# Kernel tuning notes

Measured on AMD Instinct MI355X. Metric: run time of the kernel, lower is better.

The kernel has to match this reference:

```python
import jax, jax.numpy as jnp
import numpy as np

E, S, L, H, C = 32, 64, 20, 512, 32  # episodes, steps, max_comm_len, hidden_size, comm_shape
STD_MIN, STD_MAX = 2.0611536e-09, 7.389056  # exp(-20), exp(2)


def setup_inputs() -> dict:
    key = jax.random.key(0)
    ks = jax.random.split(key, 12)
    def p(k, shape):
        return jax.random.normal(k, shape, jnp.float32) * 0.02
    return {
        'x': jax.random.normal(ks[0], (E, S, H), jnp.float32),
        'Wr': p(ks[1], (2 * H, H)), 'br': jnp.zeros((H,), jnp.float32),
        'Wz': p(ks[2], (2 * H, H)), 'bz': jnp.zeros((H,), jnp.float32),
        'Wn': p(ks[3], (2 * H, H)), 'bn': jnp.zeros((H,), jnp.float32),
        'conv_w1': p(ks[4], (H // 4, H, 1)), 'conv_b1': jnp.zeros((H // 4,), jnp.float32),
        'conv_w3': p(ks[5], (H // 4, H, 3)), 'conv_b3': jnp.zeros((H // 4,), jnp.float32),
        'conv_w5': p(ks[6], (H // 4, H, 5)), 'conv_b5': jnp.zeros((H // 4,), jnp.float32),
        'conv_w7': p(ks[7], (H // 4, H, 7)), 'conv_b7': jnp.zeros((H // 4,), jnp.float32),
        'prelu_a': jnp.asarray(0.25, jnp.float32),
        'W_mu': p(ks[8], (H, C)), 'b_mu': jnp.zeros((C,), jnp.float32),
        'W_std': p(ks[9], (H, C)), 'b_std': jnp.zeros((C,), jnp.float32),
        'eps': jax.random.normal(ks[10], (E, S, L, C), jnp.float32),
    }


def reference(x, Wr, br, Wz, bz, Wn, bn,
              conv_w1, conv_b1, conv_w3, conv_b3, conv_w5, conv_b5, conv_w7, conv_b7,
              prelu_a, W_mu, b_mu, W_std, b_std, eps):
    B = E * S
    xf = x.reshape(B, H)  # same input fed to the RNN at every comm step

    def step(h, _):
        xh = jnp.concatenate([xf, h], -1)
        r = jax.nn.sigmoid(xh @ Wr + br)
        z = jax.nn.sigmoid(xh @ Wz + bz)
        n = jnp.tanh(jnp.concatenate([xf, r * h], -1) @ Wn + bn)
        h_new = (1.0 - z) * n + z * h  # time_constant=1 -> h = new GRU state
        return h_new, h_new

    h0 = jnp.zeros((B, H), x.dtype)
    _, hs = jax.lax.scan(step, h0, None, length=L)  # (L, B, H)
    comm_h = jnp.transpose(hs, (1, 2, 0))  # (B, H, L) -- NCW layout for conv

    dn = ('NCH', 'OIH', 'NCH')
    def conv(w, b, k):
        pad = (k - 1) // 2
        y = jax.lax.conv_general_dilated(comm_h, w, (1,), [(pad, pad)], dimension_numbers=dn)
        return y + b[None, :, None]

    y = jnp.concatenate([
        conv(conv_w1, conv_b1, 1),
        conv(conv_w3, conv_b3, 3),
        conv(conv_w5, conv_b5, 5),
        conv(conv_w7, conv_b7, 7),
    ], axis=1)  # (B, H, L)
    y = jnp.where(y >= 0, y, prelu_a * y)  # PReLU; dropout is identity in eval
    y = jnp.transpose(y, (0, 2, 1)).reshape(E, S, L, H)

    mu = y @ W_mu + b_mu
    std = jnp.clip(jax.nn.softplus(y @ W_std + b_std), STD_MIN, STD_MAX)
    comm = mu + eps * std  # reparameterized Normal sample
    comm_out = jnp.tanh(comm)
    log2pi = jnp.asarray(np.log(2.0 * np.pi), jnp.float32)
    log_prob = (-0.5 * ((comm - mu) / std) ** 2 - jnp.log(std) - 0.5 * log2pi
                - jnp.log(1.0 - comm_out ** 2 + 1e-6))
    log_prob = jnp.mean(log_prob, -1, keepdims=True)  # (E,S,L,1)
    log_prob = jnp.mean(log_prob, -2)  # (E,S,1)
    return comm_out, log_prob
```

## Files before the change

kernel.cpp:

```cpp
#include <hip/hip_runtime.h>
#include <hip/hip_bf16.h>

typedef __hip_bfloat16 bf16;
typedef short short8 __attribute__((ext_vector_type(8)));
typedef float floatx4 __attribute__((ext_vector_type(4)));

#define BDIM 2048
#define HDIM 512
#define LDIM 20
#define CDIM 32
#define LSTR 40

__device__ __forceinline__ float sigm(float x) { return 1.0f / (1.0f + expf(-x)); }

__device__ __forceinline__ void ll16(const short* g, short* l)
{
    __builtin_amdgcn_global_load_lds(
        (const __attribute__((address_space(1))) void*)g,
        (__attribute__((address_space(3))) void*)l, 16, 0, 0);
}
#define WAITVM(N) asm volatile("s_waitcnt vmcnt(" #N ")" ::: "memory")

__device__ __forceinline__ void gemm_tile_k(
    const short* __restrict__ A, int lda,
    const short* __restrict__ Bt, int ldb,
    int K, short* lds, floatx4 (&acc)[4][4], int tid)
{
    short* As = lds;
    short* Bs = lds + 128 * LSTR;
    const int wave = tid >> 6, lane = tid & 63;
    const int wm = wave & 1, wn = wave >> 1;
    const int m16 = lane & 15, quad = lane >> 4;
    const int r0 = tid >> 2;
    const int koff = (tid & 3) * 8;

    short8 a0 = *(const short8*)(A + (size_t)r0 * lda + koff);
    short8 a1 = *(const short8*)(A + (size_t)(r0 + 64) * lda + koff);
    short8 b0 = *(const short8*)(Bt + (size_t)r0 * ldb + koff);
    short8 b1 = *(const short8*)(Bt + (size_t)(r0 + 64) * ldb + koff);
    for (int k0 = 0; k0 < K; k0 += 32) {
        __syncthreads();
        *(short8*)(As + r0 * LSTR + koff) = a0;
        *(short8*)(As + (r0 + 64) * LSTR + koff) = a1;
        *(short8*)(Bs + r0 * LSTR + koff) = b0;
        *(short8*)(Bs + (r0 + 64) * LSTR + koff) = b1;
        __syncthreads();
        if (k0 + 32 < K) {
            a0 = *(const short8*)(A + (size_t)r0 * lda + k0 + 32 + koff);
            a1 = *(const short8*)(A + (size_t)(r0 + 64) * lda + k0 + 32 + koff);
            b0 = *(const short8*)(Bt + (size_t)r0 * ldb + k0 + 32 + koff);
            b1 = *(const short8*)(Bt + (size_t)(r0 + 64) * ldb + k0 + 32 + koff);
        }
        short8 af[4], bfr[4];
#pragma unroll
        for (int i = 0; i < 4; ++i)
            af[i] = *(short8*)(As + (wm * 64 + i * 16 + m16) * LSTR + quad * 8);
#pragma unroll
        for (int j = 0; j < 4; ++j)
            bfr[j] = *(short8*)(Bs + (wn * 64 + j * 16 + m16) * LSTR + quad * 8);
#pragma unroll
        for (int i = 0; i < 4; ++i)
#pragma unroll
            for (int j = 0; j < 4; ++j)
                acc[i][j] = __builtin_amdgcn_mfma_f32_16x16x32_bf16(
                    af[i], bfr[j], acc[i][j], 0, 0, 0);
    }
}

__device__ __forceinline__ void gemm_tile_k256(
    const short* __restrict__ A,
    const short* __restrict__ Bt,
    short* lds, floatx4 (&acc)[4][4], int tid)
{
    short* As = lds;
    short* Bs = lds + 256 * LSTR;
    const int wave = tid >> 6, lane = tid & 63;
    const int wm = wave & 3, wn = wave >> 2;
    const int m16 = lane & 15, quad = lane >> 4;
    const int r0 = tid >> 2;
    const int koff = (tid & 3) * 8;

    short8 a0 = *(const short8*)(A + (size_t)r0 * 512 + koff);
    short8 a1 = *(const short8*)(A + (size_t)(r0 + 128) * 512 + koff);
    short8 b0 = *(const short8*)(Bt + (size_t)r0 * 512 + koff);
    for (int k0 = 0; k0 < 512; k0 += 32) {
        __syncthreads();
        *(short8*)(As + r0 * LSTR + koff) = a0;
        *(short8*)(As + (r0 + 128) * LSTR + koff) = a1;
        *(short8*)(Bs + r0 * LSTR + koff) = b0;
        __syncthreads();
        if (k0 + 32 < 512) {
            a0 = *(const short8*)(A + (size_t)r0 * 512 + k0 + 32 + koff);
            a1 = *(const short8*)(A + (size_t)(r0 + 128) * 512 + k0 + 32 + koff);
            b0 = *(const short8*)(Bt + (size_t)r0 * 512 + k0 + 32 + koff);
        }
        short8 af[4], bfr[4];
#pragma unroll
        for (int i = 0; i < 4; ++i)
            af[i] = *(short8*)(As + (wm * 64 + i * 16 + m16) * LSTR + quad * 8);
#pragma unroll
        for (int j = 0; j < 4; ++j)
            bfr[j] = *(short8*)(Bs + (wn * 64 + j * 16 + m16) * LSTR + quad * 8);
#pragma unroll
        for (int i = 0; i < 4; ++i)
#pragma unroll
            for (int j = 0; j < 4; ++j)
                acc[i][j] = __builtin_amdgcn_mfma_f32_16x16x32_bf16(
                    af[i], bfr[j], acc[i][j], 0, 0, 0);
    }
}

__global__ __launch_bounds__(256) void k_prep_xb(const float* __restrict__ x,
                                                 bf16* __restrict__ xb)
{
    int i = blockIdx.x * 256 + threadIdx.x;
    xb[i] = (bf16)x[i];
}

__global__ __launch_bounds__(256) void k_transpose_512(const float* __restrict__ src,
                                                       bf16* __restrict__ dst)
{
    __shared__ float tile[32][33];
    int tx = threadIdx.x & 31, ty = threadIdx.x >> 5;
    int k0 = blockIdx.x * 32, n0 = blockIdx.y * 32;
#pragma unroll
    for (int i = 0; i < 32; i += 8)
        tile[ty + i][tx] = src[(size_t)(k0 + ty + i) * 512 + n0 + tx];
    __syncthreads();
#pragma unroll
    for (int i = 0; i < 32; i += 8)
        dst[(size_t)(n0 + ty + i) * 512 + k0 + tx] = (bf16)tile[tx][ty + i];
}

__global__ __launch_bounds__(256) void k_swzW(const float* __restrict__ Wr,
                                              const float* __restrict__ Wz,
                                              const float* __restrict__ Wn,
                                              bf16* __restrict__ Wfrag)
{
    int idx = blockIdx.x * 256 + threadIdx.x;
    int e = idx & 7, lane = (idx >> 3) & 63;
    int t2 = idx >> 9;
    int f = t2 % 6, jk = t2 / 6;
    int kc = jk & 15, j = jk >> 4;
    int ftype = f >> 1;
    int col = j * 32 + (f & 1) * 16 + (lane & 15);
    int k = kc * 32 + ((lane >> 4) << 3) + e;
    const float* W = (ftype == 0) ? Wr : (ftype == 1) ? Wz : Wn;
    Wfrag[idx] = (bf16)W[(size_t)(512 + k) * 512 + col];
}

__global__ __launch_bounds__(256) void k_prep_wc(
    const float* __restrict__ w1, const float* __restrict__ w3,
    const float* __restrict__ w5, const float* __restrict__ w7,
    bf16* __restrict__ wt)
{
    int idx = blockIdx.x * 256 + threadIdx.x;
    int g, base;
    if (idx < 65536)       { g = 0; base = 0;      }
    else if (idx < 262144) { g = 1; base = 65536;  }
    else if (idx < 589824) { g = 2; base = 262144; }
    else                   { g = 3; base = 589824; }
    int rel = idx - base;
    int k = 2 * g + 1;
    int ci = rel & 511;
    int t2 = rel >> 9;
    int co = t2 & 127;
    int tap = t2 >> 7;
    const float* w = (g == 0) ? w1 : (g == 1) ? w3 : (g == 2) ? w5 : w7;
    wt[idx] = (bf16)w[((size_t)co * 512 + ci) * k + tap];
}

__global__ __launch_bounds__(256) void k_prep_wh(const float* __restrict__ Wmu,
                                                 const float* __restrict__ Wstd,
                                                 bf16* __restrict__ Wh_t)
{
    int idx = blockIdx.x * 256 + threadIdx.x;
    int n = idx >> 9, k = idx & 511;
    float v = (n < 32) ? Wmu[(size_t)k * 32 + n] : Wstd[(size_t)k * 32 + (n - 32)];
    Wh_t[idx] = (bf16)v;
}

__global__ __launch_bounds__(256) void k_gx(
    const bf16* __restrict__ xb, const bf16* __restrict__ Wx_t,
    const float* __restrict__ br, const float* __restrict__ bz,
    const float* __restrict__ bn, bf16* __restrict__ gxb)
{
    __shared__ short lds[2 * 128 * LSTR];
    const int tid = threadIdx.x;
    const int row0 = blockIdx.x * 128, col0 = blockIdx.y * 128;
    floatx4 acc[4][4];
#pragma unroll
    for (int i = 0; i < 4; ++i)
#pragma unroll
        for (int j = 0; j < 4; ++j) acc[i][j] = (floatx4)0.0f;
    gemm_tile_k((const short*)xb + (size_t)row0 * 512, 512,
                (const short*)Wx_t + (size_t)col0 * 512, 512, 512, lds, acc, tid);
    const int wave = tid >> 6, lane = tid & 63;
    const int wm = wave & 1, wn = wave >> 1;
    const int m16 = lane & 15, quad = lane >> 4;
#pragma unroll
    for (int i = 0; i < 4; ++i)
#pragma unroll
        for (int j = 0; j < 4; ++j)
#pragma unroll
            for (int reg = 0; reg < 4; ++reg) {
                int b = row0 + wm * 64 + i * 16 + quad * 4 + reg;
                int n = col0 + wn * 64 + j * 16 + m16;
                float bias = (n < 512) ? br[n] : (n < 1024) ? bz[n - 512] : bn[n - 1024];
                gxb[(size_t)b * 1536 + n] = (bf16)(acc[i][j][reg] + bias);
            }
}

__device__ __forceinline__ void gbar2(unsigned* flags, int j, unsigned target,
                                      bool fast, int tid)
{
    WAITVM(0);
    __syncthreads();
    if (tid < 64) {
        if (tid == 0) {
            if (!fast) __threadfence();
            __hip_atomic_store(flags + j, target, __ATOMIC_RELAXED,
                               __HIP_MEMORY_SCOPE_AGENT);
        }
        unsigned v; int guard = 0;
        do {
            v = (tid < 16) ? __hip_atomic_load(flags + tid, __ATOMIC_RELAXED,
                                               __HIP_MEMORY_SCOPE_AGENT)
                           : target;
        } while (__ballot(v >= target) != ~0ull && ++guard < (1 << 20));
        if (!fast) { if (tid == 0) __threadfence(); }
        else asm volatile("buffer_inv" ::: "memory");
    }
    __syncthreads();
}

template<int NF>
__device__ __forceinline__ void phase_reg(
    const short* __restrict__ srcw, const short* __restrict__ wl,
    int f0, int lane, floatx4 (&acc)[NF])
{
    const short* g = srcw + (size_t)(lane & 15) * 512 + (lane >> 4) * 8;
    short8 a[16];
#pragma unroll
    for (int kc = 0; kc < 16; ++kc)
        a[kc] = *(const short8*)(g + kc * 32);
#pragma unroll
    for (int kc = 0; kc < 16; ++kc) {
        short8 bfr[NF];
#pragma unroll
        for (int f = 0; f < NF; ++f)
            bfr[f] = *(short8*)(wl + ((kc * 6 + f0 + f) << 9) + lane * 8);
#pragma unroll
        for (int f = 0; f < NF; ++f)
            acc[f] = __builtin_amdgcn_mfma_f32_16x16x32_bf16(a[kc], bfr[f],
                                                             acc[f], 0, 0, 0);
    }
}

__global__ __launch_bounds__(512, 2) void k_gru9(
    const bf16* __restrict__ Wfrag, const bf16* __restrict__ gxb,
    bf16* __restrict__ hs, bf16* __restrict__ rhb,
    unsigned* __restrict__ ctr, int* __restrict__ xcdtab)
{
    __shared__ short wlds[6 * 16 * 512];
    const int tid = threadIdx.x;
    const int wave = tid >> 6, lane = tid & 63;
    const int m16 = lane & 15, quad = lane >> 4;
    const int b = blockIdx.x;
    const int s = b >> 3;
    const int m = (b & 7) + ((s & 1) << 3);
    const int j = s >> 1;
    const int wrow = wave * 16;
    unsigned* flg  = ctr + m * 32;
    unsigned* vflg = ctr + m * 32 + 16;

    int myxcd;
    asm volatile("s_getreg_b32 %0, hwreg(HW_REG_XCC_ID)" : "=s"(myxcd));
    myxcd &= 15;
    if (tid == 0) xcdtab[m * 16 + j] = myxcd;

    const short* wsrc = (const short*)Wfrag + (size_t)j * 49152;
#pragma unroll
    for (int r = 0; r < 12; ++r)
        ll16(wsrc + ((wave * 12 + r) << 9) + lane * 8, wlds + ((wave * 12 + r) << 9));

    float gxr[2][4], gxz[2][4], gxn[2][4];
#pragma unroll
    for (int reg = 0; reg < 4; ++reg) {
        const bf16* gp = gxb + (size_t)(m * 128 + wrow + quad * 4 + reg) * 1536 + j * 32;
#pragma unroll
        for (int fc = 0; fc < 2; ++fc) {
            int c = fc * 16 + m16;
            gxr[fc][reg] = __bfloat162float(gp[c]);
            gxz[fc][reg] = __bfloat162float(gp[512 + c]);
            gxn[fc][reg] = __bfloat162float(gp[1024 + c]);
        }
    }

    gbar2(vflg, j, 1u, false, tid);
    bool fast = true;
#pragma unroll
    for (int jj = 0; jj < 16; ++jj) {
        int xv = __hip_atomic_load((const int*)xcdtab + m * 16 + jj,
                                   __ATOMIC_RELAXED, __HIP_MEMORY_SCOPE_AGENT);
        fast = fast && (xv == myxcd);
    }

    float h32[2][4];
    float zf[2][4];
    unsigned nbar = 0;
    const int rowg = m * 128 + wrow + quad * 4;

#pragma unroll
    for (int fc = 0; fc < 2; ++fc)
#pragma unroll
        for (int reg = 0; reg < 4; ++reg) {
            float z = sigm(gxz[fc][reg]);
            float nv = tanhf(gxn[fc][reg]);
            float hn = (1.0f - z) * nv;
            h32[fc][reg] = hn;
            hs[(size_t)(rowg + reg) * 512 + j * 32 + fc * 16 + m16] = (bf16)hn;
        }
    ++nbar; gbar2(flg, j, nbar, fast, tid);

    for (int t = 1; t < LDIM; ++t) {
        floatx4 acc[4];
#pragma unroll
        for (int f = 0; f < 4; ++f) acc[f] = (floatx4)0.0f;
        phase_reg<4>((const short*)hs + ((size_t)(t - 1) * BDIM + m * 128 + wrow) * 512,
                     wlds, 0, lane, acc);
#pragma unroll
        for (int fc = 0; fc < 2; ++fc)
#pragma unroll
            for (int reg = 0; reg < 4; ++reg) {
                float r = sigm(acc[fc][reg] + gxr[fc][reg]);
                zf[fc][reg] = sigm(acc[2 + fc][reg] + gxz[fc][reg]);
                rhb[(size_t)(rowg + reg) * 512 + j * 32 + fc * 16 + m16] =
                    (bf16)(r * h32[fc][reg]);
            }
        ++nbar; gbar2(flg, j, nbar, fast, tid);
        floatx4 acc2[2];
#pragma unroll
        for (int f = 0; f < 2; ++f) acc2[f] = (floatx4)0.0f;
        phase_reg<2>((const short*)rhb + (size_t)(m * 128 + wrow) * 512,
                     wlds, 4, lane, acc2);
#pragma unroll
        for (int fc = 0; fc < 2; ++fc)
#pragma unroll
            for (int reg = 0; reg < 4; ++reg) {
                float nv = tanhf(acc2[fc][reg] + gxn[fc][reg]);
                float z = zf[fc][reg];
                float hn = (1.0f - z) * nv + z * h32[fc][reg];
                h32[fc][reg] = hn;
                hs[((size_t)t * BDIM + rowg + reg) * 512 + j * 32 + fc * 16 + m16] =
                    (bf16)hn;
            }
        if (t < LDIM - 1) { ++nbar; gbar2(flg, j, nbar, fast, tid); }
    }
}

__global__ __launch_bounds__(512, 2) void k_conv(
    const bf16* __restrict__ hs, const bf16* __restrict__ Wc_t,
    const float* __restrict__ b1, const float* __restrict__ b3,
    const float* __restrict__ b5, const float* __restrict__ b7,
    const float* __restrict__ pa, bf16* __restrict__ y)
{
    __shared__ short lds[(256 + 128) * LSTR];
    const int tid = threadIdx.x;
    const int btile = blockIdx.x, g = blockIdx.y, l = blockIdx.z;
    const int row0 = btile * 256;
    const int ktap = 2 * g + 1, p = g;
    const int offs[4] = {0, 65536, 262144, 589824};
    const short* Wg = (const short*)Wc_t + offs[g];
    floatx4 acc[4][4];
#pragma unroll
    for (int i = 0; i < 4; ++i)
#pragma unroll
        for (int j = 0; j < 4; ++j) acc[i][j] = (floatx4)0.0f;
    for (int tap = 0; tap < ktap; ++tap) {
        int li = l + tap - p;
        if (li < 0 || li >= LDIM) continue;
        gemm_tile_k256((const short*)hs + (size_t)li * BDIM * HDIM + (size_t)row0 * 512,
                       Wg + (size_t)tap * 128 * 512, lds, acc, tid);
    }
    const float* bp = (g == 0) ? b1 : (g == 1) ? b3 : (g == 2) ? b5 : b7;
    const float a = *pa;
    const int wave = tid >> 6, lane = tid & 63;
    const int wm = wave & 3, wn = wave >> 2;
    const int m16 = lane & 15, quad = lane >> 4;
#pragma unroll
    for (int i = 0; i < 4; ++i)
#pragma unroll
        for (int j = 0; j < 4; ++j)
#pragma unroll
            for (int reg = 0; reg < 4; ++reg) {
                int b = row0 + wm * 64 + i * 16 + quad * 4 + reg;
                int col = wn * 64 + j * 16 + m16;
                float v = acc[i][j][reg] + bp[col];
                v = (v >= 0.0f) ? v : a * v;
                y[((size_t)b * LDIM + l) * 512 + g * 128 + col] = (bf16)v;
            }
}

__global__ __launch_bounds__(256) void k_head2(
    const bf16* __restrict__ y, const bf16* __restrict__ Wh_t,
    const float* __restrict__ bmu, const float* __restrict__ bstd,
    const float* __restrict__ eps, float* __restrict__ out_comm,
    float* __restrict__ lpsum)
{
    __shared__ short As[128 * LSTR];
    __shared__ short Bs[64 * LSTR];
    const int tid = threadIdx.x;
    const int wave = tid >> 6, lane = tid & 63;
    const int m16 = lane & 15, quad = lane >> 4;
    const int r0 = tid >> 2, koff = (tid & 3) * 8;
    const int row0 = blockIdx.x * 128;
    floatx4 acc[2][4];
#pragma unroll
    for (int i = 0; i < 2; ++i)
#pragma unroll
        for (int j = 0; j < 4; ++j) acc[i][j] = (floatx4)0.0f;
    const short* Ap = (const short*)y + (size_t)row0 * 512;
    const short* Bp = (const short*)Wh_t;
    short8 ga0 = *(const short8*)(Ap + (size_t)r0 * 512 + koff);
    short8 ga1 = *(const short8*)(Ap + (size_t)(r0 + 64) * 512 + koff);
    short8 gb0 = *(const short8*)(Bp + (size_t)r0 * 512 + koff);
    for (int k0 = 0; k0 < 512; k0 += 32) {
        __syncthreads();
        *(short8*)(As + r0 * LSTR + koff) = ga0;
        *(short8*)(As + (r0 + 64) * LSTR + koff) = ga1;
        *(short8*)(Bs + r0 * LSTR + koff) = gb0;
        __syncthreads();
        if (k0 + 32 < 512) {
            ga0 = *(const short8*)(Ap + (size_t)r0 * 512 + k0 + 32 + koff);
            ga1 = *(const short8*)(Ap + (size_t)(r0 + 64) * 512 + k0 + 32 + koff);
            gb0 = *(const short8*)(Bp + (size_t)r0 * 512 + k0 + 32 + koff);
        }
        short8 af[2], bfr[4];
#pragma unroll
        for (int i = 0; i < 2; ++i)
            af[i] = *(short8*)(As + (wave * 32 + i * 16 + m16) * LSTR + quad * 8);
#pragma unroll
        for (int j = 0; j < 4; ++j)
            bfr[j] = *(short8*)(Bs + (j * 16 + m16) * LSTR + quad * 8);
#pragma unroll
        for (int i = 0; i < 2; ++i)
#pragma unroll
            for (int j = 0; j < 4; ++j)
                acc[i][j] = __builtin_amdgcn_mfma_f32_16x16x32_bf16(
                    af[i], bfr[j], acc[i][j], 0, 0, 0);
    }
#pragma unroll
    for (int i = 0; i < 2; ++i)
#pragma unroll
        for (int reg = 0; reg < 4; ++reg) {
            int row = row0 + wave * 32 + i * 16 + quad * 4 + reg;
            float lp = 0.0f;
#pragma unroll
            for (int jj = 0; jj < 2; ++jj) {
                int c = jj * 16 + m16;
                float mu = acc[i][jj][reg] + bmu[c];
                float sraw = acc[i][jj + 2][reg] + bstd[c];
                float sp = (sraw > 20.0f) ? sraw : log1pf(expf(sraw));
                float sd = fminf(fmaxf(sp, 2.0611536e-09f), 7.389056f);
                float e = eps[(size_t)row * 32 + c];
                float comm = fmaf(e, sd, mu);
                float tt = tanhf(comm);
                out_comm[(size_t)row * 32 + c] = tt;
                lp += -0.5f * e * e - logf(sd) - 0.91893853320467274f
                      - logf(1.0f - tt * tt + 1e-6f);
            }
            lp += __shfl_xor(lp, 1, 16);
            lp += __shfl_xor(lp, 2, 16);
            lp += __shfl_xor(lp, 4, 16);
            lp += __shfl_xor(lp, 8, 16);
            if (m16 == 0) lpsum[row] = lp;
        }
}

__global__ __launch_bounds__(256) void k_final(const float* __restrict__ lpsum,
                                               float* __restrict__ out2)
{
    int b = blockIdx.x * 256 + threadIdx.x;
    if (b < BDIM) {
        float s = 0.0f;
#pragma unroll
        for (int i = 0; i < LDIM; ++i) s += lpsum[b * LDIM + i];
        out2[b] = s * (1.0f / (LDIM * CDIM));
    }
}

extern "C" void kernel_launch(void* const* d_in, const int* in_sizes, int n_in,
                              void* d_out, int out_size, void* d_ws, size_t ws_size,
                              hipStream_t stream)
{
    const float* x    = (const float*)d_in[0];
    const float* Wr   = (const float*)d_in[1];
    const float* br   = (const float*)d_in[2];
    const float* Wz   = (const float*)d_in[3];
    const float* bz   = (const float*)d_in[4];
    const float* Wn   = (const float*)d_in[5];
    const float* bn   = (const float*)d_in[6];
    const float* w1   = (const float*)d_in[7];
    const float* b1   = (const float*)d_in[8];
    const float* w3   = (const float*)d_in[9];
    const float* b3   = (const float*)d_in[10];
    const float* w5   = (const float*)d_in[11];
    const float* b5   = (const float*)d_in[12];
    const float* w7   = (const float*)d_in[13];
    const float* b7   = (const float*)d_in[14];
    const float* pa   = (const float*)d_in[15];
    const float* Wmu  = (const float*)d_in[16];
    const float* bmu  = (const float*)d_in[17];
    const float* Wstd = (const float*)d_in[18];
    const float* bstd = (const float*)d_in[19];
    const float* eps  = (const float*)d_in[20];

    char* cur = (char*)d_ws;
    auto alloc = [&](size_t bytes) -> void* {
        void* r = (void*)cur;
        cur += (bytes + 255) & ~(size_t)255;
        return r;
    };
    const size_t BH = (size_t)BDIM * HDIM;
    bf16*  gxb   = (bf16*)alloc((size_t)BDIM * 1536 * 2);
    bf16*  xb    = (bf16*)alloc(BH * 2);
    bf16*  hs    = (bf16*)alloc(BH * LDIM * 2);
    bf16*  ybuf  = (bf16*)alloc(BH * LDIM * 2);
    bf16*  Wx_t  = (bf16*)alloc((size_t)1536 * 512 * 2);
    bf16*  Wfrag = (bf16*)alloc((size_t)786432 * 2);
    bf16*  Wc_t  = (bf16*)alloc((size_t)1048576 * 2);
    bf16*  Wh_t  = (bf16*)alloc((size_t)64 * 512 * 2);
    bf16*  rhb   = (bf16*)alloc((size_t)BDIM * 512 * 2);
    float* lpsum = (float*)alloc((size_t)BDIM * LDIM * 4);
    unsigned* ctr = (unsigned*)alloc(2048);
    int*   xcdtab = (int*)alloc(1024);

    hipMemsetAsync(ctr, 0, 2048, stream);

    k_prep_xb<<<4096, 256, 0, stream>>>(x, xb);
    dim3 tg(16, 16);
    k_transpose_512<<<tg, 256, 0, stream>>>(Wr, Wx_t);
    k_transpose_512<<<tg, 256, 0, stream>>>(Wz, Wx_t + 262144);
    k_transpose_512<<<tg, 256, 0, stream>>>(Wn, Wx_t + 524288);
    k_swzW<<<3072, 256, 0, stream>>>(Wr, Wz, Wn, Wfrag);
    k_prep_wc<<<4096, 256, 0, stream>>>(w1, w3, w5, w7, Wc_t);
    k_prep_wh<<<128, 256, 0, stream>>>(Wmu, Wstd, Wh_t);

    k_gx<<<dim3(16, 12), 256, 0, stream>>>(xb, Wx_t, br, bz, bn, gxb);

    k_gru9<<<256, 512, 0, stream>>>(Wfrag, gxb, hs, rhb, ctr, xcdtab);

    k_conv<<<dim3(8, 4, 20), 512, 0, stream>>>(hs, Wc_t, b1, b3, b5, b7, pa, ybuf);

    float* out_comm = (float*)d_out;
    float* out_lp   = (float*)d_out + (size_t)BDIM * LDIM * CDIM;
    k_head2<<<320, 256, 0, stream>>>(ybuf, Wh_t, bmu, bstd, eps, out_comm, lpsum);
    k_final<<<8, 256, 0, stream>>>(lpsum, out_lp);
}
```

Baseline: 537.9 us.

## Replace block-wide GRU barriers with per-wave flag barriers across row groups

The GRU recurrence kernel no longer uses block-level __syncthreads plus a single flag line per row group. Each wave now publishes and polls its own 16-entry flag line, so a wave waits only on the 16 column blocks that produce its 16 rows, with s_sleep backoff while polling. This removes intra-block stalls and lets waves proceed independently, at the cost of more flag traffic and a larger flag area. The conv launch is also flattened from a 3D grid to a 1D grid, which changes the order in which blocks are dispatched.

```diff
diff --git a/kernel.cpp b/kernel.cpp
--- a/kernel.cpp
+++ b/kernel.cpp
@@ -211,25 +211,47 @@
             }
 }
 
-__device__ __forceinline__ void gbar2(unsigned* flags, int j, unsigned target,
-                                      bool fast, int tid)
+__device__ __forceinline__ void wbar(unsigned* line, int j, unsigned target,
+                                     bool fast, int lane)
+{
+    WAITVM(0);
+    if (!fast) __threadfence();
+    if (lane == 0)
+        __hip_atomic_store(line + j, target, __ATOMIC_RELAXED,
+                           __HIP_MEMORY_SCOPE_AGENT);
+    unsigned v = target;
+    int guard = 0;
+    for (;;) {
+        if (lane < 16)
+            v = __hip_atomic_load(line + lane, __ATOMIC_RELAXED,
+                                  __HIP_MEMORY_SCOPE_AGENT);
+        if (__ballot(v >= target) == ~0ull) break;
+        if (++guard >= (1 << 20)) break;
+        __builtin_amdgcn_s_sleep(1);
+    }
+    if (!fast) __threadfence();
+    else asm volatile("buffer_inv" ::: "memory");
+    __builtin_amdgcn_sched_barrier(0);
+}
+
+__device__ __forceinline__ void gbar_verify(unsigned* flags, int j,
+                                            unsigned target, int tid)
 {
     WAITVM(0);
     __syncthreads();
     if (tid < 64) {
         if (tid == 0) {
-            if (!fast) __threadfence();
+            __threadfence();
             __hip_atomic_store(flags + j, target, __ATOMIC_RELAXED,
                                __HIP_MEMORY_SCOPE_AGENT);
         }
-        unsigned v; int guard = 0;
+        unsigned v = target; int guard = 0;
         do {
             v = (tid < 16) ? __hip_atomic_load(flags + tid, __ATOMIC_RELAXED,
                                                __HIP_MEMORY_SCOPE_AGENT)
                            : target;
         } while (__ballot(v >= target) != ~0ull && ++guard < (1 << 20));
-        if (!fast) { if (tid == 0) __threadfence(); }
-        else asm volatile("buffer_inv" ::: "memory");
+        if (tid == 0) __threadfence();
     }
     __syncthreads();
 }
@@ -257,10 +279,10 @@
     }
 }
 
-__global__ __launch_bounds__(512, 2) void k_gru9(
+__global__ __launch_bounds__(512, 2) void k_gru12(
     const bf16* __restrict__ Wfrag, const bf16* __restrict__ gxb,
     bf16* __restrict__ hs, bf16* __restrict__ rhb,
-    unsigned* __restrict__ ctr, int* __restrict__ xcdtab)
+    unsigned* __restrict__ flags, int* __restrict__ xcdtab)
 {
     __shared__ short wlds[6 * 16 * 512];
     const int tid = threadIdx.x;
@@ -271,8 +293,7 @@
     const int m = (b & 7) + ((s & 1) << 3);
     const int j = s >> 1;
     const int wrow = wave * 16;
-    unsigned* flg  = ctr + m * 32;
-    unsigned* vflg = ctr + m * 32 + 16;
+    unsigned* wline = flags + (m * 8 + wave) * 16;
 
     int myxcd;
     asm volatile("s_getreg_b32 %0, hwreg(HW_REG_XCC_ID)" : "=s"(myxcd));
@@ -297,7 +318,7 @@
         }
     }
 
-    gbar2(vflg, j, 1u, false, tid);
+    gbar_verify(flags + 8192 + m * 32, j, 1u, tid);
     bool fast = true;
 #pragma unroll
     for (int jj = 0; jj < 16; ++jj) {
@@ -321,7 +342,7 @@
             h32[fc][reg] = hn;
             hs[(size_t)(rowg + reg) * 512 + j * 32 + fc * 16 + m16] = (bf16)hn;
         }
-    ++nbar; gbar2(flg, j, nbar, fast, tid);
+    ++nbar; wbar(wline, j, nbar, fast, lane);
 
     for (int t = 1; t < LDIM; ++t) {
         floatx4 acc[4];
@@ -338,7 +359,7 @@
                 rhb[(size_t)(rowg + reg) * 512 + j * 32 + fc * 16 + m16] =
                     (bf16)(r * h32[fc][reg]);
             }
-        ++nbar; gbar2(flg, j, nbar, fast, tid);
+        ++nbar; wbar(wline, j, nbar, fast, lane);
         floatx4 acc2[2];
 #pragma unroll
         for (int f = 0; f < 2; ++f) acc2[f] = (floatx4)0.0f;
@@ -355,7 +376,7 @@
                 hs[((size_t)t * BDIM + rowg + reg) * 512 + j * 32 + fc * 16 + m16] =
                     (bf16)hn;
             }
-        if (t < LDIM - 1) { ++nbar; gbar2(flg, j, nbar, fast, tid); }
+        if (t < LDIM - 1) { ++nbar; wbar(wline, j, nbar, fast, lane); }
     }
 }
 
@@ -367,7 +388,10 @@
 {
     __shared__ short lds[(256 + 128) * LSTR];
     const int tid = threadIdx.x;
-    const int btile = blockIdx.x, g = blockIdx.y, l = blockIdx.z;
+    const int bidx = blockIdx.x;
+    const int btile = bidx & 7;
+    const int yy = bidx >> 3;
+    const int g = yy & 3, l = yy >> 2;
     const int row0 = btile * 256;
     const int ktap = 2 * g + 1, p = g;
     const int offs[4] = {0, 65536, 262144, 589824};
@@ -533,10 +557,10 @@
     bf16*  Wh_t  = (bf16*)alloc((size_t)64 * 512 * 2);
     bf16*  rhb   = (bf16*)alloc((size_t)BDIM * 512 * 2);
     float* lpsum = (float*)alloc((size_t)BDIM * LDIM * 4);
-    unsigned* ctr = (unsigned*)alloc(2048);
+    unsigned* flags = (unsigned*)alloc(65536);
     int*   xcdtab = (int*)alloc(1024);
 
-    hipMemsetAsync(ctr, 0, 2048, stream);
+    hipMemsetAsync(flags, 0, 65536, stream);
 
     k_prep_xb<<<4096, 256, 0, stream>>>(x, xb);
     dim3 tg(16, 16);
@@ -549,9 +573,9 @@
 
     k_gx<<<dim3(16, 12), 256, 0, stream>>>(xb, Wx_t, br, bz, bn, gxb);
 
-    k_gru9<<<256, 512, 0, stream>>>(Wfrag, gxb, hs, rhb, ctr, xcdtab);
-
-    k_conv<<<dim3(8, 4, 20), 512, 0, stream>>>(hs, Wc_t, b1, b3, b5, b7, pa, ybuf);
+    k_gru12<<<256, 512, 0, stream>>>(Wfrag, gxb, hs, rhb, flags, xcdtab);
+
+    k_conv<<<640, 512, 0, stream>>>(hs, Wc_t, b1, b3, b5, b7, pa, ybuf);
 
     float* out_comm = (float*)d_out;
     float* out_lp   = (float*)d_out + (size_t)BDIM * LDIM * CDIM;
```

After: 823.6 us. +53.1%, slower.

## Replace GRU grid barriers with per-chunk flag gating and shrink conv tiles

Applied to the files above, without the earlier changes.

In the persistent GRU kernel, when all cooperating blocks share one XCD, the full barrier after each phase becomes a publish-only flag store. Each wave then waits only on the producer flag for each K-chunk just before loading that chunk, so loads and MFMAs can start before every peer has finished. The conv kernel moves from 256x128 tiles with 512 threads to 128x128 tiles with 256 threads, doubling the block count for better occupancy. The finer-grained sync relies on relaxed atomics and buffer_inv for visibility, and the spin guard is lowered.

```diff
diff --git a/kernel.cpp b/kernel.cpp
--- a/kernel.cpp
+++ b/kernel.cpp
@@ -67,49 +67,6 @@
     }
 }
 
-__device__ __forceinline__ void gemm_tile_k256(
-    const short* __restrict__ A,
-    const short* __restrict__ Bt,
-    short* lds, floatx4 (&acc)[4][4], int tid)
-{
-    short* As = lds;
-    short* Bs = lds + 256 * LSTR;
-    const int wave = tid >> 6, lane = tid & 63;
-    const int wm = wave & 3, wn = wave >> 2;
-    const int m16 = lane & 15, quad = lane >> 4;
-    const int r0 = tid >> 2;
-    const int koff = (tid & 3) * 8;
-
-    short8 a0 = *(const short8*)(A + (size_t)r0 * 512 + koff);
-    short8 a1 = *(const short8*)(A + (size_t)(r0 + 128) * 512 + koff);
-    short8 b0 = *(const short8*)(Bt + (size_t)r0 * 512 + koff);
-    for (int k0 = 0; k0 < 512; k0 += 32) {
-        __syncthreads();
-        *(short8*)(As + r0 * LSTR + koff) = a0;
-        *(short8*)(As + (r0 + 128) * LSTR + koff) = a1;
-        *(short8*)(Bs + r0 * LSTR + koff) = b0;
-        __syncthreads();
-        if (k0 + 32 < 512) {
-            a0 = *(const short8*)(A + (size_t)r0 * 512 + k0 + 32 + koff);
-            a1 = *(const short8*)(A + (size_t)(r0 + 128) * 512 + k0 + 32 + koff);
-            b0 = *(const short8*)(Bt + (size_t)r0 * 512 + k0 + 32 + koff);
-        }
-        short8 af[4], bfr[4];
-#pragma unroll
-        for (int i = 0; i < 4; ++i)
-            af[i] = *(short8*)(As + (wm * 64 + i * 16 + m16) * LSTR + quad * 8);
-#pragma unroll
-        for (int j = 0; j < 4; ++j)
-            bfr[j] = *(short8*)(Bs + (wn * 64 + j * 16 + m16) * LSTR + quad * 8);
-#pragma unroll
-        for (int i = 0; i < 4; ++i)
-#pragma unroll
-            for (int j = 0; j < 4; ++j)
-                acc[i][j] = __builtin_amdgcn_mfma_f32_16x16x32_bf16(
-                    af[i], bfr[j], acc[i][j], 0, 0, 0);
-    }
-}
-
 __global__ __launch_bounds__(256) void k_prep_xb(const float* __restrict__ x,
                                                  bf16* __restrict__ xb)
 {
@@ -227,11 +184,20 @@
             v = (tid < 16) ? __hip_atomic_load(flags + tid, __ATOMIC_RELAXED,
                                                __HIP_MEMORY_SCOPE_AGENT)
                            : target;
-        } while (__ballot(v >= target) != ~0ull && ++guard < (1 << 20));
+        } while (__ballot(v >= target) != ~0ull && ++guard < (1 << 18));
         if (!fast) { if (tid == 0) __threadfence(); }
         else asm volatile("buffer_inv" ::: "memory");
     }
     __syncthreads();
+}
+
+__device__ __forceinline__ void publish(unsigned* flg, int j, unsigned val)
+{
+    WAITVM(0);
+    __syncthreads();
+    if (threadIdx.x == 0)
+        __hip_atomic_store(flg + j, val, __ATOMIC_RELAXED,
+                           __HIP_MEMORY_SCOPE_AGENT);
 }
 
 template<int NF>
@@ -257,7 +223,51 @@
     }
 }
 
-__global__ __launch_bounds__(512, 2) void k_gru9(
+template<int NF>
+__device__ __forceinline__ void phase_gated(
+    const short* __restrict__ srcw, const short* __restrict__ wl,
+    int f0, int lane, unsigned* flg, unsigned target, bool do_inv,
+    floatx4 (&acc)[NF])
+{
+    unsigned v = target;
+    if (lane < 16)
+        v = __hip_atomic_load(flg + lane, __ATOMIC_RELAXED,
+                              __HIP_MEMORY_SCOPE_AGENT);
+    unsigned long long ready = __ballot(v >= target);
+    if (do_inv) asm volatile("buffer_inv" ::: "memory");
+    __builtin_amdgcn_sched_barrier(0);
+
+    const short* g = srcw + (size_t)(lane & 15) * 512 + (lane >> 4) * 8;
+    short8 a[16];
+#pragma unroll
+    for (int kc = 0; kc < 16; ++kc) {
+        if (!((ready >> kc) & 1)) {
+            unsigned vv = __hip_atomic_load(flg + kc, __ATOMIC_RELAXED,
+                                            __HIP_MEMORY_SCOPE_AGENT);
+            int guard = 0;
+            while (vv < target && ++guard < (1 << 18)) {
+                __builtin_amdgcn_s_sleep(2);
+                vv = __hip_atomic_load(flg + kc, __ATOMIC_RELAXED,
+                                       __HIP_MEMORY_SCOPE_AGENT);
+            }
+            __builtin_amdgcn_sched_barrier(0);
+        }
+        a[kc] = *(const short8*)(g + kc * 32);
+    }
+#pragma unroll
+    for (int kc = 0; kc < 16; ++kc) {
+        short8 bfr[NF];
+#pragma unroll
+        for (int f = 0; f < NF; ++f)
+            bfr[f] = *(short8*)(wl + ((kc * 6 + f0 + f) << 9) + lane * 8);
+#pragma unroll
+        for (int f = 0; f < NF; ++f)
+            acc[f] = __builtin_amdgcn_mfma_f32_16x16x32_bf16(a[kc], bfr[f],
+                                                             acc[f], 0, 0, 0);
+    }
+}
+
+__global__ __launch_bounds__(512, 2) void k_gru13(
     const bf16* __restrict__ Wfrag, const bf16* __restrict__ gxb,
     bf16* __restrict__ hs, bf16* __restrict__ rhb,
     unsigned* __restrict__ ctr, int* __restrict__ xcdtab)
@@ -308,7 +318,6 @@
 
     float h32[2][4];
     float zf[2][4];
-    unsigned nbar = 0;
     const int rowg = m * 128 + wrow + quad * 4;
 
 #pragma unroll
@@ -321,14 +330,18 @@
             h32[fc][reg] = hn;
             hs[(size_t)(rowg + reg) * 512 + j * 32 + fc * 16 + m16] = (bf16)hn;
         }
-    ++nbar; gbar2(flg, j, nbar, fast, tid);
+    if (fast) publish(flg, j, 1u);
+    else      gbar2(flg, j, 1u, false, tid);
 
     for (int t = 1; t < LDIM; ++t) {
+        const unsigned tg1 = 2 * t - 1, tg2 = 2 * t;
         floatx4 acc[4];
 #pragma unroll
         for (int f = 0; f < 4; ++f) acc[f] = (floatx4)0.0f;
-        phase_reg<4>((const short*)hs + ((size_t)(t - 1) * BDIM + m * 128 + wrow) * 512,
-                     wlds, 0, lane, acc);
+        const short* h_src = (const short*)hs +
+            ((size_t)(t - 1) * BDIM + m * 128 + wrow) * 512;
+        if (fast) phase_gated<4>(h_src, wlds, 0, lane, flg, tg1, false, acc);
+        else      phase_reg<4>(h_src, wlds, 0, lane, acc);
 #pragma unroll
         for (int fc = 0; fc < 2; ++fc)
 #pragma unroll
@@ -338,12 +351,14 @@
                 rhb[(size_t)(rowg + reg) * 512 + j * 32 + fc * 16 + m16] =
                     (bf16)(r * h32[fc][reg]);
             }
-        ++nbar; gbar2(flg, j, nbar, fast, tid);
+        if (fast) publish(flg, j, tg2);
+        else      gbar2(flg, j, tg2, false, tid);
         floatx4 acc2[2];
 #pragma unroll
         for (int f = 0; f < 2; ++f) acc2[f] = (floatx4)0.0f;
-        phase_reg<2>((const short*)rhb + (size_t)(m * 128 + wrow) * 512,
-                     wlds, 4, lane, acc2);
+        const short* rh_src = (const short*)rhb + (size_t)(m * 128 + wrow) * 512;
+        if (fast) phase_gated<2>(rh_src, wlds, 4, lane, flg, tg2, true, acc2);
+        else      phase_reg<2>(rh_src, wlds, 4, lane, acc2);
 #pragma unroll
         for (int fc = 0; fc < 2; ++fc)
 #pragma unroll
@@ -355,20 +370,23 @@
                 hs[((size_t)t * BDIM + rowg + reg) * 512 + j * 32 + fc * 16 + m16] =
                     (bf16)hn;
             }
-        if (t < LDIM - 1) { ++nbar; gbar2(flg, j, nbar, fast, tid); }
-    }
-}
-
-__global__ __launch_bounds__(512, 2) void k_conv(
+        if (t < LDIM - 1) {
+            if (fast) publish(flg, j, tg2 + 1);
+            else      gbar2(flg, j, tg2 + 1, false, tid);
+        }
+    }
+}
+
+__global__ __launch_bounds__(256) void k_conv(
     const bf16* __restrict__ hs, const bf16* __restrict__ Wc_t,
     const float* __restrict__ b1, const float* __restrict__ b3,
     const float* __restrict__ b5, const float* __restrict__ b7,
     const float* __restrict__ pa, bf16* __restrict__ y)
 {
-    __shared__ short lds[(256 + 128) * LSTR];
+    __shared__ short lds[2 * 128 * LSTR];
     const int tid = threadIdx.x;
     const int btile = blockIdx.x, g = blockIdx.y, l = blockIdx.z;
-    const int row0 = btile * 256;
+    const int row0 = btile * 128;
     const int ktap = 2 * g + 1, p = g;
     const int offs[4] = {0, 65536, 262144, 589824};
     const short* Wg = (const short*)Wc_t + offs[g];
@@ -380,13 +398,13 @@
     for (int tap = 0; tap < ktap; ++tap) {
         int li = l + tap - p;
         if (li < 0 || li >= LDIM) continue;
-        gemm_tile_k256((const short*)hs + (size_t)li * BDIM * HDIM + (size_t)row0 * 512,
-                       Wg + (size_t)tap * 128 * 512, lds, acc, tid);
+        gemm_tile_k((const short*)hs + (size_t)li * BDIM * HDIM + (size_t)row0 * 512, 512,
+                    Wg + (size_t)tap * 128 * 512, 512, 512, lds, acc, tid);
     }
     const float* bp = (g == 0) ? b1 : (g == 1) ? b3 : (g == 2) ? b5 : b7;
     const float a = *pa;
     const int wave = tid >> 6, lane = tid & 63;
-    const int wm = wave & 3, wn = wave >> 2;
+    const int wm = wave & 1, wn = wave >> 1;
     const int m16 = lane & 15, quad = lane >> 4;
 #pragma unroll
     for (int i = 0; i < 4; ++i)
@@ -549,9 +567,9 @@
 
     k_gx<<<dim3(16, 12), 256, 0, stream>>>(xb, Wx_t, br, bz, bn, gxb);
 
-    k_gru9<<<256, 512, 0, stream>>>(Wfrag, gxb, hs, rhb, ctr, xcdtab);
-
-    k_conv<<<dim3(8, 4, 20), 512, 0, stream>>>(hs, Wc_t, b1, b3, b5, b7, pa, ybuf);
+    k_gru13<<<256, 512, 0, stream>>>(Wfrag, gxb, hs, rhb, ctr, xcdtab);
+
+    k_conv<<<dim3(16, 4, 20), 256, 0, stream>>>(hs, Wc_t, b1, b3, b5, b7, pa, ybuf);
 
     float* out_comm = (float*)d_out;
     float* out_lp   = (float*)d_out + (size_t)BDIM * LDIM * CDIM;
```

New measurement: 568.6 us. +5.7%, slower.
